# Performance work log

Measured on AMD Instinct MI355X. Metric: run time of the kernel, lower is better.

Reference implementation:

```python
import jax, jax.numpy as jnp
import numpy as np

T_SEG = 8  # n_segment


def _layer_norm(x, eps=1e-5):
    # F.layer_norm over last dim, no affine (torch default eps=1e-5)
    mu = x.mean(-1, keepdims=True)
    var = ((x - mu) ** 2).mean(-1, keepdims=True)
    return (x - mu) / jnp.sqrt(var + eps)


def setup_inputs() -> dict:
    key = jax.random.key(0)
    k1, k2, k3 = jax.random.split(key, 3)
    B, T, C, H, W = 8, T_SEG, 512, 56, 56
    R = C // 4  # rsize = in_channels // n_div
    x = jax.random.normal(k1, (B * T, C, H, W), jnp.float32)
    W_down = jax.random.normal(k2, (R, C), jnp.float32) / np.sqrt(C).astype(np.float32)
    b_down = jnp.zeros((R,), jnp.float32)
    W_up = jax.random.normal(k3, (C, R), jnp.float32) / np.sqrt(R).astype(np.float32)
    b_up = jnp.zeros((C,), jnp.float32)
    return {"x": x, "W_down": W_down, "b_down": b_down, "W_up": W_up, "b_up": b_up}


def reference(x, W_down, b_down, W_up, b_up):
    t = T_SEG
    shortcut = x
    # conv_down: 1x1 conv == per-pixel GEMM
    h = jnp.einsum('bchw,oc->bohw', x, W_down) + b_down[None, :, None, None]
    bt, c, H, W = h.shape
    b = bt // t

    def to_attn(z):  # (b t) c h w -> (b h w) t c
        return z.reshape(b, t, c, H, W).transpose(0, 3, 4, 1, 2).reshape(b * H * W, t, c)

    def from_attn(z):  # (b h w) t c -> (b t) c h w
        return z.reshape(b, H, W, t, c).transpose(0, 3, 4, 1, 2).reshape(bt, c, H, W)

    # LayerNorm over channel dim (last dim of attn layout)
    xn = from_attn(_layer_norm(to_attn(h)))

    # Motion: rearrange to (b, t, c, h, w), shift-left along dim 3 (h), subtract
    z = xn.reshape(b, t, c, H, W)
    shifted = jnp.concatenate([z[:, :, :, 1:], jnp.zeros_like(z[:, :, :, :1])], axis=3)
    xn = (shifted - z).reshape(bt, c, H, W)

    # raw bmm self-attention with q = k = v
    q = to_attn(xn)  # ((b h w), t, c)
    scores = jax.nn.softmax(
        jnp.einsum('btc,bsc->bts', q, q) / jnp.sqrt(jnp.float32(c)), axis=-1)
    attn = jnp.einsum('bts,bsc->btc', scores, q)

    h = from_attn(attn) + h  # residual inside attention block

    # conv_up + sigmoid gate + residual
    up = jnp.einsum('bchw,oc->bohw', h, W_up) + b_up[None, :, None, None]
    gate = jax.nn.sigmoid(up)
    return gate * shortcut + shortcut
```

## Files before the change

### kernel.cpp

```cpp
#include <hip/hip_runtime.h>
#include <cstdint>
#include <cstddef>

#define HW   3136
#define WROW 56
#define CIN  512
#define RMID 128
#define HWQ  196

typedef unsigned int  u32;
typedef unsigned short u16;
typedef __attribute__((ext_vector_type(8))) short s16x8;
typedef __attribute__((ext_vector_type(4))) float f32x4;

__device__ __forceinline__ u16 f2bf(float f) {
    u32 u = __float_as_uint(f);
    u32 r = u + 0x7fffu + ((u >> 16) & 1u);
    return (u16)(r >> 16);
}
__device__ __forceinline__ float bf2f(u32 bits16) {
    return __uint_as_float(bits16 << 16);
}
__device__ __forceinline__ u32 pk2(float a, float b) {
    return (u32)f2bf(a) | ((u32)f2bf(b) << 16);
}

__global__ __launch_bounds__(256) void kprep(
    const float* __restrict__ Wd, const float* __restrict__ Wu,
    u16* __restrict__ wdf, u16* __restrict__ wuf)
{
    const int t = blockIdx.x * 256 + threadIdx.x;
    const int l = t & 63, g = t >> 6;
    const int lo = l & 15, hi = l >> 4;
    const float* src;
    u16* dst;
    if (g < 128) {
        const int s = g >> 3, m = g & 7;
        src = Wd + (size_t)(m * 16 + lo) * CIN + s * 32 + hi * 8;
        dst = wdf + (size_t)t * 8;
    } else {
        const int g2 = g - 128;
        const int mt = g2 >> 2, s = g2 & 3;
        src = Wu + (size_t)(mt * 16 + lo) * RMID + s * 32 + hi * 8;
        dst = wuf + (size_t)(t - 8192) * 8;
    }
    float4 a = *(const float4*)src;
    float4 b = *(const float4*)(src + 4);
    uint4 o;
    o.x = pk2(a.x, a.y); o.y = pk2(a.z, a.w);
    o.z = pk2(b.x, b.y); o.w = pk2(b.z, b.w);
    *(uint4*)dst = o;
}

__global__ __launch_bounds__(256) void k1_down_ln(
    const float* __restrict__ x, const u16* __restrict__ wdf,
    const float* __restrict__ bd, u16* __restrict__ hd,
    float* __restrict__ st)
{
    __shared__ u16 xl[128 * 40];

    const int tid  = threadIdx.x;
    const int lane = tid & 63, w = tid >> 6;
    const int h = blockIdx.x;
    const int slot = h >> 3;
    const int bt = (h & 7) * 8 + slot / 25;
    const int px0 = (slot % 25) * 128;
    const int b = bt >> 3, t = bt & 7;

    const int pxp2 = px0 + 2 * lane;
    const int pxa = (pxp2 > HW - 2) ? (HW - 2) : pxp2;
    const float* xb = x + (size_t)bt * CIN * HW + pxa;

    const int p16 = lane & 15, lg = lane >> 4;

    f32x4 acc[8][2];
    const f32x4 zz = {0.f, 0.f, 0.f, 0.f};
#pragma unroll
    for (int m = 0; m < 8; ++m) { acc[m][0] = zz; acc[m][1] = zz; }

    for (int s = 0; s < 16; ++s) {
        const float* xs = xb + (size_t)(s * 32 + w * 8) * HW;
        float2 v[8];
#pragma unroll
        for (int j = 0; j < 8; ++j)
            v[j] = *(const float2*)(xs + (size_t)j * HW);
        uint4 pkA, pkB;
        pkA.x = pk2(v[0].x, v[1].x); pkA.y = pk2(v[2].x, v[3].x);
        pkA.z = pk2(v[4].x, v[5].x); pkA.w = pk2(v[6].x, v[7].x);
        pkB.x = pk2(v[0].y, v[1].y); pkB.y = pk2(v[2].y, v[3].y);
        pkB.z = pk2(v[4].y, v[5].y); pkB.w = pk2(v[6].y, v[7].y);
        *(uint4*)&xl[(size_t)(2 * lane)     * 40 + w * 8] = pkA;
        *(uint4*)&xl[(size_t)(2 * lane + 1) * 40 + w * 8] = pkB;
        __syncthreads();
        s16x8 bf0 = *(const s16x8*)&xl[(w * 32 +      p16) * 40 + lg * 8];
        s16x8 bf1 = *(const s16x8*)&xl[(w * 32 + 16 + p16) * 40 + lg * 8];
#pragma unroll
        for (int m = 0; m < 8; ++m) {
            s16x8 af = *(const s16x8*)(wdf + ((size_t)((s * 8 + m) * 64 + lane)) * 8);
            acc[m][0] = __builtin_amdgcn_mfma_f32_16x16x32_bf16(af, bf0, acc[m][0], 0, 0, 0);
            acc[m][1] = __builtin_amdgcn_mfma_f32_16x16x32_bf16(af, bf1, acc[m][1], 0, 0, 0);
        }
        __syncthreads();
    }

#pragma unroll
    for (int n = 0; n < 2; ++n) {
        const int hwpx = px0 + w * 32 + n * 16 + p16;
        const bool ok = hwpx < HW;
        float sum = 0.f, sq = 0.f;
        const size_t hbase = ((size_t)(b * HW + (ok ? hwpx : 0)) * 8 + t) * 128 + lg * 4;
#pragma unroll
        for (int m = 0; m < 8; ++m) {
            float4 bv = *(const float4*)(bd + m * 16 + lg * 4);
            float v0 = acc[m][n].x + bv.x;
            float v1 = acc[m][n].y + bv.y;
            float v2 = acc[m][n].z + bv.z;
            float v3 = acc[m][n].w + bv.w;
            sum += v0 + v1 + v2 + v3;
            sq  += v0*v0 + v1*v1 + v2*v2 + v3*v3;
            if (ok) {
                ushort4 o;
                o.x = f2bf(v0); o.y = f2bf(v1); o.z = f2bf(v2); o.w = f2bf(v3);
                *(ushort4*)(hd + hbase + m * 16) = o;
            }
        }
        sum += __shfl_xor(sum, 16); sum += __shfl_xor(sum, 32);
        sq  += __shfl_xor(sq, 16);  sq  += __shfl_xor(sq, 32);
        if (ok && lg == 0) {
            float mu  = sum * (1.f / 128.f);
            float var = sq  * (1.f / 128.f) - mu * mu;
            float2 s2 = make_float2(mu, rsqrtf(var + 1e-5f));
            *(float2*)(st + ((size_t)(b * HW + hwpx) * 8 + t) * 2) = s2;
        }
    }
}

__global__ __launch_bounds__(256) void k2a_attn(
    const u16* __restrict__ hd, const float* __restrict__ st,
    u16* __restrict__ h2f)
{
    __shared__ float ql[4][8 * 132];
    __shared__ float pl[4][8][9];

    const int tid = threadIdx.x, wid = tid >> 6, lane = tid & 63;
    const int P = blockIdx.x * 4 + wid;
    const int b = P / HW;
    const int hw = P - b * HW;
    const int hrow = hw / WROW;
    const bool hasnext = hrow < (WROW - 1);

    const u16* cur = hd + (size_t)P * 1024;
    const int tq = lane >> 3, cbase = (lane & 7) * 16;

    uint4 c0 = *(const uint4*)(cur + tq * 128 + cbase);
    uint4 c1 = *(const uint4*)(cur + tq * 128 + cbase + 8);
    float2 ms = *(const float2*)(st + ((size_t)P * 8 + tq) * 2);

    float hv[16];
    hv[0]=bf2f(c0.x&0xffff); hv[1]=bf2f(c0.x>>16); hv[2]=bf2f(c0.y&0xffff); hv[3]=bf2f(c0.y>>16);
    hv[4]=bf2f(c0.z&0xffff); hv[5]=bf2f(c0.z>>16); hv[6]=bf2f(c0.w&0xffff); hv[7]=bf2f(c0.w>>16);
    hv[8]=bf2f(c1.x&0xffff); hv[9]=bf2f(c1.x>>16); hv[10]=bf2f(c1.y&0xffff); hv[11]=bf2f(c1.y>>16);
    hv[12]=bf2f(c1.z&0xffff); hv[13]=bf2f(c1.z>>16); hv[14]=bf2f(c1.w&0xffff); hv[15]=bf2f(c1.w>>16);

    float qv[16];
    if (hasnext) {
        const u16* nx = cur + (size_t)WROW * 1024;
        uint4 n0 = *(const uint4*)(nx + tq * 128 + cbase);
        uint4 n1 = *(const uint4*)(nx + tq * 128 + cbase + 8);
        float2 mn = *(const float2*)(st + ((size_t)(P + WROW) * 8 + tq) * 2);
        float nv[16];
        nv[0]=bf2f(n0.x&0xffff); nv[1]=bf2f(n0.x>>16); nv[2]=bf2f(n0.y&0xffff); nv[3]=bf2f(n0.y>>16);
        nv[4]=bf2f(n0.z&0xffff); nv[5]=bf2f(n0.z>>16); nv[6]=bf2f(n0.w&0xffff); nv[7]=bf2f(n0.w>>16);
        nv[8]=bf2f(n1.x&0xffff); nv[9]=bf2f(n1.x>>16); nv[10]=bf2f(n1.y&0xffff); nv[11]=bf2f(n1.y>>16);
        nv[12]=bf2f(n1.z&0xffff); nv[13]=bf2f(n1.z>>16); nv[14]=bf2f(n1.w&0xffff); nv[15]=bf2f(n1.w>>16);
#pragma unroll
        for (int i = 0; i < 16; ++i)
            qv[i] = (nv[i] - mn.x) * mn.y - (hv[i] - ms.x) * ms.y;
    } else {
#pragma unroll
        for (int i = 0; i < 16; ++i)
            qv[i] = -(hv[i] - ms.x) * ms.y;
    }

    float* qrow = &ql[wid][tq * 132 + cbase];
#pragma unroll
    for (int i = 0; i < 4; ++i)
        *(float4*)(qrow + i * 4) = make_float4(qv[4*i], qv[4*i+1], qv[4*i+2], qv[4*i+3]);
    __syncthreads();

    const int tt = lane >> 3, ss = lane & 7;
    const float* qt = &ql[wid][tt * 132];
    const float* qs = &ql[wid][ss * 132];
    float dot = 0.f;
#pragma unroll 8
    for (int c4 = 0; c4 < 32; ++c4) {
        float4 a4 = *(const float4*)(qt + c4 * 4);
        float4 g4 = *(const float4*)(qs + c4 * 4);
        dot += a4.x*g4.x + a4.y*g4.y + a4.z*g4.z + a4.w*g4.w;
    }
    dot *= 0.08838834764831845f;
    float mx = dot;
    mx = fmaxf(mx, __shfl_xor(mx, 1));
    mx = fmaxf(mx, __shfl_xor(mx, 2));
    mx = fmaxf(mx, __shfl_xor(mx, 4));
    float e = __expf(dot - mx);
    float sm = e;
    sm += __shfl_xor(sm, 1); sm += __shfl_xor(sm, 2); sm += __shfl_xor(sm, 4);
    pl[wid][tt][ss] = e / sm;
    __syncthreads();

    float at[16];
#pragma unroll
    for (int i = 0; i < 16; ++i) at[i] = hv[i];
#pragma unroll
    for (int s = 0; s < 8; ++s) {
        float p = pl[wid][tq][s];
        const float* qsr = &ql[wid][s * 132 + cbase];
#pragma unroll
        for (int i4 = 0; i4 < 4; ++i4) {
            float4 q4 = *(const float4*)(qsr + i4 * 4);
            at[4*i4+0] += p * q4.x; at[4*i4+1] += p * q4.y;
            at[4*i4+2] += p * q4.z; at[4*i4+3] += p * q4.w;
        }
    }

    const int hwq = hw >> 4, pp = hw & 15;
    const size_t base = ((((size_t)(b * 8 + tq) * HWQ + hwq) * 16 + (cbase >> 3)) * 16 + pp) * 8;
    uint4 o0, o1;
    o0.x = pk2(at[0], at[1]);  o0.y = pk2(at[2], at[3]);
    o0.z = pk2(at[4], at[5]);  o0.w = pk2(at[6], at[7]);
    o1.x = pk2(at[8], at[9]);  o1.y = pk2(at[10], at[11]);
    o1.z = pk2(at[12], at[13]); o1.w = pk2(at[14], at[15]);
    *(uint4*)(h2f + base) = o0;
    *(uint4*)(h2f + base + 128) = o1;
}

__global__ __launch_bounds__(64, 4) void k2b_up_out(
    const u16* __restrict__ h2f, const u16* __restrict__ wuf,
    const float* __restrict__ bu, const float* __restrict__ x,
    float* __restrict__ out)
{
    __shared__ float sl[16 * 68];

    const int lane = threadIdx.x;
    const int h = blockIdx.x;
    const int slot = h >> 3;
    const int bt = (h & 7) * 8 + (slot >> 7);
    const int oc = (slot & 127) >> 2;
    const int q  = slot & 3;
    const int p16 = lane & 15, lg = lane >> 4;

    s16x8 wf[4];
#pragma unroll
    for (int s = 0; s < 4; ++s)
        wf[s] = *(const s16x8*)(wuf + ((size_t)((oc * 4 + s) * 64 + lane)) * 8);

    float bvr[4];
#pragma unroll
    for (int i = 0; i < 4; ++i) bvr[i] = bu[oc * 16 + i * 4 + lg];

    const u16* bp0 = h2f + (size_t)bt * HWQ * 2048;
    const size_t xrow = (size_t)bt * CIN * HW + (size_t)(oc * 16) * HW;

    const int ng = (q == 0) ? 13 : 12;
    for (int it = 0; it < ng; ++it) {
        const int g = (it < 12) ? (it * 4 + q) : 48;
        const int px0 = g * 64;

        float4 xv[4];
#pragma unroll
        for (int i = 0; i < 4; ++i)
            xv[i] = *(const float4*)(x + xrow + (size_t)(i * 4 + lg) * HW + px0 + p16 * 4);

#pragma unroll
        for (int tt = 0; tt < 4; ++tt) {
            const u16* bp = bp0 + (size_t)(g * 4 + tt) * 2048;
            f32x4 a = {0.f, 0.f, 0.f, 0.f};
#pragma unroll
            for (int s = 0; s < 4; ++s) {
                s16x8 af = *(const s16x8*)(bp + ((size_t)((s * 4 + lg) * 16 + p16)) * 8);
                a = __builtin_amdgcn_mfma_f32_16x16x32_bf16(af, wf[s], a, 0, 0, 0);
            }
            *(f32x4*)&sl[p16 * 68 + tt * 16 + lg * 4] = a;
        }

#pragma unroll
        for (int i = 0; i < 4; ++i) {
            const int ol = i * 4 + lg;
            f32x4 a4 = *(const f32x4*)&sl[ol * 68 + p16 * 4];
            const size_t off = xrow + (size_t)ol * HW + px0 + p16 * 4;
            float4 rr;
            rr.x = xv[i].x * (1.f + 1.f / (1.f + __expf(-(a4.x + bvr[i]))));
            rr.y = xv[i].y * (1.f + 1.f / (1.f + __expf(-(a4.y + bvr[i]))));
            rr.z = xv[i].z * (1.f + 1.f / (1.f + __expf(-(a4.z + bvr[i]))));
            rr.w = xv[i].w * (1.f + 1.f / (1.f + __expf(-(a4.w + bvr[i]))));
            *(float4*)(out + off) = rr;
        }
    }
}

extern "C" void kernel_launch(void* const* d_in, const int* in_sizes, int n_in,
                              void* d_out, int out_size, void* d_ws, size_t ws_size,
                              hipStream_t stream)
{
    (void)in_sizes; (void)n_in; (void)out_size; (void)ws_size;
    const float* x  = (const float*)d_in[0];
    const float* Wd = (const float*)d_in[1];
    const float* bd = (const float*)d_in[2];
    const float* Wu = (const float*)d_in[3];
    const float* bu = (const float*)d_in[4];
    float* out = (float*)d_out;

    char* wsp = (char*)d_ws;
    u16*  hd  = (u16*)wsp;                 wsp += 51380224;
    u16*  h2f = (u16*)wsp;                 wsp += 51380224;
    float* st = (float*)wsp;               wsp += 1605632;
    u16*  wdf = (u16*)wsp;                 wsp += 131072;
    u16*  wuf = (u16*)wsp;                 wsp += 131072;

    kprep     <<<dim3(64),   256, 0, stream>>>(Wd, Wu, wdf, wuf);
    k1_down_ln<<<dim3(1600), 256, 0, stream>>>(x, wdf, bd, hd, st);
    k2a_attn  <<<dim3(6272), 256, 0, stream>>>(hd, st, h2f);
    k2b_up_out<<<dim3(8192), 64,  0, stream>>>(h2f, wuf, bu, x, out);
}
```

Before: 420.5 us.

## Double-buffer x staging in down-projection and widen up-projection pixel tiles

In k1_down_ln, the LDS staging buffer is doubled so the global loads for the next channel slab are issued before the current slab's MFMAs, and the packed writes land in the other buffer. This removes one barrier per iteration and hides global load latency behind compute. In k2b_up_out, each block now handles 128-pixel groups with 2 quarter-splits instead of 64-pixel groups with 4, halving the grid. The tail group is handled separately and the LDS tile is widened. These give wider, fully coalesced 32-lane row stores, at the cost of more registers and lower block-level parallelism.

```diff
diff --git a/kernel.cpp b/kernel.cpp
--- a/kernel.cpp
+++ b/kernel.cpp
@@ -57,7 +57,7 @@
     const float* __restrict__ bd, u16* __restrict__ hd,
     float* __restrict__ st)
 {
-    __shared__ u16 xl[128 * 40];
+    __shared__ u16 xl[2][128 * 40];
 
     const int tid  = threadIdx.x;
     const int lane = tid & 63, w = tid >> 6;
@@ -73,33 +73,43 @@
 
     const int p16 = lane & 15, lg = lane >> 4;
 
-    f32x4 acc[8][2];
-    const f32x4 zz = {0.f, 0.f, 0.f, 0.f};
-#pragma unroll
-    for (int m = 0; m < 8; ++m) { acc[m][0] = zz; acc[m][1] = zz; }
-
-    for (int s = 0; s < 16; ++s) {
+    float2 v[8];
+    auto loads = [&](int s) {
         const float* xs = xb + (size_t)(s * 32 + w * 8) * HW;
-        float2 v[8];
 #pragma unroll
         for (int j = 0; j < 8; ++j)
             v[j] = *(const float2*)(xs + (size_t)j * HW);
+    };
+    auto packw = [&](int buf) {
         uint4 pkA, pkB;
         pkA.x = pk2(v[0].x, v[1].x); pkA.y = pk2(v[2].x, v[3].x);
         pkA.z = pk2(v[4].x, v[5].x); pkA.w = pk2(v[6].x, v[7].x);
         pkB.x = pk2(v[0].y, v[1].y); pkB.y = pk2(v[2].y, v[3].y);
         pkB.z = pk2(v[4].y, v[5].y); pkB.w = pk2(v[6].y, v[7].y);
-        *(uint4*)&xl[(size_t)(2 * lane)     * 40 + w * 8] = pkA;
-        *(uint4*)&xl[(size_t)(2 * lane + 1) * 40 + w * 8] = pkB;
-        __syncthreads();
-        s16x8 bf0 = *(const s16x8*)&xl[(w * 32 +      p16) * 40 + lg * 8];
-        s16x8 bf1 = *(const s16x8*)&xl[(w * 32 + 16 + p16) * 40 + lg * 8];
+        *(uint4*)&xl[buf][(size_t)(2 * lane)     * 40 + w * 8] = pkA;
+        *(uint4*)&xl[buf][(size_t)(2 * lane + 1) * 40 + w * 8] = pkB;
+    };
+
+    f32x4 acc[8][2];
+    const f32x4 zz = {0.f, 0.f, 0.f, 0.f};
+#pragma unroll
+    for (int m = 0; m < 8; ++m) { acc[m][0] = zz; acc[m][1] = zz; }
+
+    loads(0); packw(0);
+    __syncthreads();
+
+    for (int s = 0; s < 16; ++s) {
+        if (s < 15) loads(s + 1);
+        const u16* xbuf = xl[s & 1];
+        s16x8 bf0 = *(const s16x8*)&xbuf[(w * 32 +      p16) * 40 + lg * 8];
+        s16x8 bf1 = *(const s16x8*)&xbuf[(w * 32 + 16 + p16) * 40 + lg * 8];
 #pragma unroll
         for (int m = 0; m < 8; ++m) {
             s16x8 af = *(const s16x8*)(wdf + ((size_t)((s * 8 + m) * 64 + lane)) * 8);
             acc[m][0] = __builtin_amdgcn_mfma_f32_16x16x32_bf16(af, bf0, acc[m][0], 0, 0, 0);
             acc[m][1] = __builtin_amdgcn_mfma_f32_16x16x32_bf16(af, bf1, acc[m][1], 0, 0, 0);
         }
+        if (s < 15) packw((s + 1) & 1);
         __syncthreads();
     }
 
@@ -240,60 +250,93 @@
     const float* __restrict__ bu, const float* __restrict__ x,
     float* __restrict__ out)
 {
-    __shared__ float sl[16 * 68];
+    __shared__ float sl[16 * 136];
 
     const int lane = threadIdx.x;
     const int h = blockIdx.x;
     const int slot = h >> 3;
-    const int bt = (h & 7) * 8 + (slot >> 7);
-    const int oc = (slot & 127) >> 2;
-    const int q  = slot & 3;
+    const int bt = (h & 7) * 8 + (slot >> 6);
+    const int rem = slot & 63;
+    const int oc = rem >> 1;
+    const int q  = rem & 1;
     const int p16 = lane & 15, lg = lane >> 4;
+    const int hi = lane >> 5, l31 = lane & 31;
 
     s16x8 wf[4];
 #pragma unroll
     for (int s = 0; s < 4; ++s)
         wf[s] = *(const s16x8*)(wuf + ((size_t)((oc * 4 + s) * 64 + lane)) * 8);
 
-    float bvr[4];
-#pragma unroll
-    for (int i = 0; i < 4; ++i) bvr[i] = bu[oc * 16 + i * 4 + lg];
+    float bvr[8];
+#pragma unroll
+    for (int i = 0; i < 8; ++i) bvr[i] = bu[oc * 16 + i * 2 + hi];
 
     const u16* bp0 = h2f + (size_t)bt * HWQ * 2048;
     const size_t xrow = (size_t)bt * CIN * HW + (size_t)(oc * 16) * HW;
 
-    const int ng = (q == 0) ? 13 : 12;
-    for (int it = 0; it < ng; ++it) {
-        const int g = (it < 12) ? (it * 4 + q) : 48;
-        const int px0 = g * 64;
-
-        float4 xv[4];
-#pragma unroll
-        for (int i = 0; i < 4; ++i)
-            xv[i] = *(const float4*)(x + xrow + (size_t)(i * 4 + lg) * HW + px0 + p16 * 4);
-
-#pragma unroll
-        for (int tt = 0; tt < 4; ++tt) {
-            const u16* bp = bp0 + (size_t)(g * 4 + tt) * 2048;
+    for (int it = 0; it < 12; ++it) {
+        const int G = it * 2 + q;
+        const int px0 = G * 128;
+
+        float4 xv[8];
+#pragma unroll
+        for (int i = 0; i < 8; ++i)
+            xv[i] = *(const float4*)(x + xrow + (size_t)(i * 2 + hi) * HW + px0 + l31 * 4);
+
+#pragma unroll
+        for (int tt = 0; tt < 8; ++tt) {
+            const u16* bp = bp0 + (size_t)(G * 8 + tt) * 2048;
             f32x4 a = {0.f, 0.f, 0.f, 0.f};
 #pragma unroll
             for (int s = 0; s < 4; ++s) {
                 s16x8 af = *(const s16x8*)(bp + ((size_t)((s * 4 + lg) * 16 + p16)) * 8);
                 a = __builtin_amdgcn_mfma_f32_16x16x32_bf16(af, wf[s], a, 0, 0, 0);
             }
-            *(f32x4*)&sl[p16 * 68 + tt * 16 + lg * 4] = a;
-        }
-
-#pragma unroll
-        for (int i = 0; i < 4; ++i) {
-            const int ol = i * 4 + lg;
-            f32x4 a4 = *(const f32x4*)&sl[ol * 68 + p16 * 4];
-            const size_t off = xrow + (size_t)ol * HW + px0 + p16 * 4;
+            *(f32x4*)&sl[p16 * 136 + tt * 16 + lg * 4] = a;
+        }
+
+#pragma unroll
+        for (int i = 0; i < 8; ++i) {
+            const int ol = i * 2 + hi;
+            f32x4 a4 = *(const f32x4*)&sl[ol * 136 + l31 * 4];
+            const size_t off = xrow + (size_t)ol * HW + px0 + l31 * 4;
             float4 rr;
             rr.x = xv[i].x * (1.f + 1.f / (1.f + __expf(-(a4.x + bvr[i]))));
             rr.y = xv[i].y * (1.f + 1.f / (1.f + __expf(-(a4.y + bvr[i]))));
             rr.z = xv[i].z * (1.f + 1.f / (1.f + __expf(-(a4.z + bvr[i]))));
             rr.w = xv[i].w * (1.f + 1.f / (1.f + __expf(-(a4.w + bvr[i]))));
+            *(float4*)(out + off) = rr;
+        }
+    }
+
+    if (q == 0) {
+        const int px0 = 3072;
+        float4 xv[4];
+#pragma unroll
+        for (int i = 0; i < 4; ++i)
+            xv[i] = *(const float4*)(x + xrow + (size_t)(i * 4 + lg) * HW + px0 + p16 * 4);
+#pragma unroll
+        for (int tt = 0; tt < 4; ++tt) {
+            const u16* bp = bp0 + (size_t)(192 + tt) * 2048;
+            f32x4 a = {0.f, 0.f, 0.f, 0.f};
+#pragma unroll
+            for (int s = 0; s < 4; ++s) {
+                s16x8 af = *(const s16x8*)(bp + ((size_t)((s * 4 + lg) * 16 + p16)) * 8);
+                a = __builtin_amdgcn_mfma_f32_16x16x32_bf16(af, wf[s], a, 0, 0, 0);
+            }
+            *(f32x4*)&sl[p16 * 136 + tt * 16 + lg * 4] = a;
+        }
+#pragma unroll
+        for (int i = 0; i < 4; ++i) {
+            const int ol = i * 4 + lg;
+            const float bv = bu[oc * 16 + ol];
+            f32x4 a4 = *(const f32x4*)&sl[ol * 136 + p16 * 4];
+            const size_t off = xrow + (size_t)ol * HW + px0 + p16 * 4;
+            float4 rr;
+            rr.x = xv[i].x * (1.f + 1.f / (1.f + __expf(-(a4.x + bv))));
+            rr.y = xv[i].y * (1.f + 1.f / (1.f + __expf(-(a4.y + bv))));
+            rr.z = xv[i].z * (1.f + 1.f / (1.f + __expf(-(a4.z + bv))));
+            rr.w = xv[i].w * (1.f + 1.f / (1.f + __expf(-(a4.w + bv))));
             *(float4*)(out + off) = rr;
         }
     }
@@ -321,5 +364,5 @@
     kprep     <<<dim3(64),   256, 0, stream>>>(Wd, Wu, wdf, wuf);
     k1_down_ln<<<dim3(1600), 256, 0, stream>>>(x, wdf, bd, hd, st);
     k2a_attn  <<<dim3(6272), 256, 0, stream>>>(hd, st, h2f);
-    k2b_up_out<<<dim3(8192), 64,  0, stream>>>(h2f, wuf, bu, x, out);
-}
+    k2b_up_out<<<dim3(4096), 64,  0, stream>>>(h2f, wuf, bu, x, out);
+}
```

New measurement: 446.9 us. +6.3%, slower.
